# Performance work log

Hardware: AMD Instinct MI355X
Metric: run time of the kernel (lower is better)

The kernel has to match this reference:

```python
import jax, jax.numpy as jnp
import numpy as np

C = 256
NH, NL, NP_ = 8, 3, 4
HD = C // NH
NLAYERS = 6


def sine_pos(H, W, num_feats=128, temperature=10000.0, eps=1e-6):
    # mmdet SinePositionalEncoding with normalize=True and an all-zero padding mask:
    # cumsum of ones -> (i+1), normalized by last element (H or W) * 2*pi.
    scale = 2.0 * np.pi
    y = (jnp.arange(1, H + 1, dtype=jnp.float32) / (H + eps)) * scale
    x = (jnp.arange(1, W + 1, dtype=jnp.float32) / (W + eps)) * scale
    d = jnp.arange(num_feats, dtype=jnp.float32)
    dim_t = temperature ** (2.0 * jnp.floor(d / 2.0) / num_feats)

    def interleave(p):  # p: (n, num_feats) -> sin on even dims, cos on odd dims, interleaved
        return jnp.stack([jnp.sin(p[:, 0::2]), jnp.cos(p[:, 1::2])], axis=-1).reshape(p.shape[0], -1)

    py = interleave(y[:, None] / dim_t)  # (H, num_feats)
    px = interleave(x[:, None] / dim_t)  # (W, num_feats)
    pos = jnp.concatenate([jnp.broadcast_to(py[:, None, :], (H, W, num_feats)),
                           jnp.broadcast_to(px[None, :, :], (H, W, num_feats))], axis=-1)
    return pos.reshape(H * W, 2 * num_feats)


def ref_points(H, W):
    # normalized pixel centers, (x, y) order, shape (H*W, 2)
    ry = (jnp.arange(H, dtype=jnp.float32) + 0.5) / H
    rx = (jnp.arange(W, dtype=jnp.float32) + 0.5) / W
    gy, gx = jnp.meshgrid(ry, rx, indexing='ij')
    return jnp.stack([gx.ravel(), gy.ravel()], axis=-1)


def ln(x, w, b, eps=1e-5):
    m = x.mean(-1, keepdims=True)
    v = x.var(-1, keepdims=True)
    return (x - m) / jnp.sqrt(v + eps) * w + b


def gnorm(x, w, b, groups=32, eps=1e-5):
    B, Ch, H, W = x.shape
    xg = x.reshape(B, groups, Ch // groups, H, W)
    m = xg.mean((2, 3, 4), keepdims=True)
    v = xg.var((2, 3, 4), keepdims=True)
    xg = (xg - m) / jnp.sqrt(v + eps)
    return xg.reshape(B, Ch, H, W) * w[None, :, None, None] + b[None, :, None, None]


def conv3x3(x, w):
    return jax.lax.conv_general_dilated(x, w, (1, 1), 'SAME',
                                        dimension_numbers=('NCHW', 'OIHW', 'NCHW'))


def ms_deform(value, shapes, loc, aw):
    # value (B,S,NH,HD); loc (B,L,NH,NL,NP,2) normalized [0,1]; aw (B,L,NH,NL,NP)
    # Matches F.grid_sample(..., align_corners=False, padding_mode='zeros').
    B, S, nH, hd = value.shape
    Lq, nP = loc.shape[1], loc.shape[4]
    out = jnp.zeros((B, Lq, nH, hd), value.dtype)
    start = 0
    for lvl, (H, W) in enumerate(shapes):
        v = value[:, start:start + H * W].transpose(0, 2, 1, 3)  # (B,nH,HW,hd)
        start += H * W
        l = loc[:, :, :, lvl]                 # (B,Lq,nH,nP,2)
        px = l[..., 0] * W - 0.5
        py = l[..., 1] * H - 0.5
        x0 = jnp.floor(px); y0 = jnp.floor(py)
        lx = px - x0; ly = py - y0
        x0i = x0.astype(jnp.int32); y0i = y0.astype(jnp.int32)

        def tw(w_):  # (B,Lq,nH,nP) -> (B,nH,Lq*nP,1)
            return w_.transpose(0, 2, 1, 3).reshape(B, nH, Lq * nP, 1)

        def gather(xi, yi):
            valid = ((xi >= 0) & (xi < W) & (yi >= 0) & (yi < H)).astype(value.dtype)
            idx = jnp.clip(yi, 0, H - 1) * W + jnp.clip(xi, 0, W - 1)
            idx = idx.transpose(0, 2, 1, 3).reshape(B, nH, Lq * nP)
            g = jnp.take_along_axis(v, idx[..., None], axis=2)  # (B,nH,Lq*nP,hd)
            return g * tw(valid)

        samp = (gather(x0i, y0i) * tw((1 - lx) * (1 - ly))
                + gather(x0i + 1, y0i) * tw(lx * (1 - ly))
                + gather(x0i, y0i + 1) * tw((1 - lx) * ly)
                + gather(x0i + 1, y0i + 1) * tw(lx * ly))
        samp = samp.reshape(B, nH, Lq, nP, hd)
        out = out + jnp.einsum('bqhp,bhqpd->bqhd', aw[:, :, :, lvl], samp)
    return out.reshape(B, Lq, nH * hd)


def _forward(feat0, feat1, feat2, in0_w, in0_b, in1_w, in1_b, in2_w, in2_b,
             off_w, off_b, aw_w, aw_b, vp_w, vp_b, op_w, op_b,
             n1_w, n1_b, ff1_w, ff1_b, ff2_w, ff2_b, n2_w, n2_b,
             fn_w, fn_b, lat_w, lat_b, out_w, gnw, gnb):
    feats = [feat0, feat1, feat2]
    in_ws = [in0_w, in1_w, in2_w]; in_bs = [in0_b, in1_b, in2_b]
    B = feat0.shape[0]
    mlvl = [jnp.einsum('oi,bihw->bohw', w, f) + b[None, :, None, None]
            for f, w, b in zip(feats, in_ws, in_bs)]
    shapes = [(f.shape[2], f.shape[3]) for f in mlvl]
    src = jnp.concatenate([f.reshape(B, C, -1).transpose(0, 2, 1) for f in mlvl], axis=1)  # (B,L,C)
    pos = jnp.concatenate([sine_pos(H, W) for (H, W) in shapes], axis=0)[None]  # (1,L,C)
    ref = jnp.concatenate([ref_points(H, W) for (H, W) in shapes], axis=0)      # (L,2)
    L = ref.shape[0]
    ref = jnp.broadcast_to(ref[None, :, None, :], (B, L, NL, 2))
    norm = jnp.array([[w_, h_] for (h_, w_) in shapes], dtype=src.dtype)  # (NL,2) = (W,H)
    for i in range(NLAYERS):
        q = src + pos
        off = (q @ off_w[i].T + off_b[i]).reshape(B, L, NH, NL, NP_, 2)
        aw = jax.nn.softmax((q @ aw_w[i].T + aw_b[i]).reshape(B, L, NH, NL * NP_), axis=-1)
        aw = aw.reshape(B, L, NH, NL, NP_)
        value = (src @ vp_w[i].T + vp_b[i]).reshape(B, L, NH, HD)
        loc = ref[:, :, None, :, None, :] + off / norm[None, None, None, :, None, :]
        attn = ms_deform(value, shapes, loc, aw) @ op_w[i].T + op_b[i]
        src = ln(src + attn, n1_w[i], n1_b[i])
        ff = jax.nn.relu(src @ ff1_w[i].T + ff1_b[i]) @ ff2_w[i].T + ff2_b[i]
        src = ln(src + ff, n2_w[i], n2_b[i])
    src = ln(src, fn_w, fn_b)
    mems, s = [], 0
    for (H, W) in shapes:
        mems.append(src[:, s:s + H * W].transpose(0, 2, 1).reshape(B, C, H, W))
        s += H * W
    mf = jnp.einsum('oi,bihw->bohw', lat_w, mems[0]) + lat_b[None, :, None, None]
    for i in range(3):
        mf = jax.nn.relu(gnorm(conv3x3(mf, out_w[i]), gnw[i], gnb[i]))
    return (mf, mems[0], mems[1], mems[2])


def setup_inputs():
    ks = iter(jax.random.split(jax.random.key(0), 64))

    def rn(shape, s=0.02):
        return jax.random.normal(next(ks), shape, dtype=jnp.float32) * s

    return dict(
        feat0=rn((1, 256, 64, 64), 1.0),
        feat1=rn((1, 512, 32, 32), 1.0),
        feat2=rn((1, 1024, 16, 16), 1.0),
        in0_w=rn((256, 256)), in0_b=rn((256,)),
        in1_w=rn((256, 512)), in1_b=rn((256,)),
        in2_w=rn((256, 1024)), in2_b=rn((256,)),
        off_w=rn((6, 192, 256), 0.002), off_b=rn((6, 192), 0.5),
        aw_w=rn((6, 96, 256)), aw_b=jnp.zeros((6, 96), jnp.float32),
        vp_w=rn((6, 256, 256)), vp_b=rn((6, 256)),
        op_w=rn((6, 256, 256)), op_b=rn((6, 256)),
        n1_w=jnp.ones((6, 256), jnp.float32), n1_b=jnp.zeros((6, 256), jnp.float32),
        ff1_w=rn((6, 1024, 256)), ff1_b=rn((6, 1024)),
        ff2_w=rn((6, 256, 1024)), ff2_b=rn((6, 256)),
        n2_w=jnp.ones((6, 256), jnp.float32), n2_b=jnp.zeros((6, 256), jnp.float32),
        fn_w=jnp.ones((256,), jnp.float32), fn_b=jnp.zeros((256,), jnp.float32),
        lat_w=rn((256, 256)), lat_b=rn((256,)),
        out_w=rn((3, 256, 256, 3, 3)),
        gnw=jnp.ones((3, 256), jnp.float32), gnb=jnp.zeros((3, 256), jnp.float32),
    )


def reference(feat0, feat1, feat2, in0_w, in0_b, in1_w, in1_b, in2_w, in2_b,
              off_w, off_b, aw_w, aw_b, vp_w, vp_b, op_w, op_b,
              n1_w, n1_b, ff1_w, ff1_b, ff2_w, ff2_b, n2_w, n2_b,
              fn_w, fn_b, lat_w, lat_b, out_w, gnw, gnb):
    return _forward(feat0, feat1, feat2, in0_w, in0_b, in1_w, in1_b, in2_w, in2_b,
                    off_w, off_b, aw_w, aw_b, vp_w, vp_b, op_w, op_b,
                    n1_w, n1_b, ff1_w, ff1_b, ff2_w, ff2_b, n2_w, n2_b,
                    fn_w, fn_b, lat_w, lat_b, out_w, gnw, gnb)
```

## Files before the change

### kernel.cpp

```cpp
#include <hip/hip_runtime.h>
#include <math.h>

#define LTOT 5376

typedef __attribute__((ext_vector_type(8))) __bf16 bf16x8;
typedef __attribute__((ext_vector_type(4))) float f32x4;
typedef __attribute__((ext_vector_type(8))) unsigned short us8;
typedef __attribute__((ext_vector_type(4))) unsigned short us4;

static __device__ __forceinline__ float4 ld4(const float* p) { return *(const float4*)p; }

static __device__ __forceinline__ unsigned short f2bf(float f) {
    unsigned int u = __float_as_uint(f);
    return (unsigned short)((u + 0x7fffu + ((u >> 16) & 1u)) >> 16);
}
static __device__ __forceinline__ float bf2f(unsigned short s) {
    return __uint_as_float(((unsigned int)s) << 16);
}

static __device__ __forceinline__ void gl16(const unsigned short* g, unsigned short* l) {
    __builtin_amdgcn_global_load_lds(
        (const __attribute__((address_space(1))) unsigned int*)g,
        (__attribute__((address_space(3))) unsigned int*)l, 16, 0, 0);
}

template<int OMODE, bool RELU>
__global__ __launch_bounds__(256) void bgemm_k(
    const unsigned short* __restrict__ A,
    const unsigned short* __restrict__ B,
    const float* __restrict__ bias,
    float* __restrict__ C1,
    unsigned short* __restrict__ C2,
    int M, int N, int K)
{
    __shared__ unsigned short As[2][64 * 64];
    __shared__ unsigned short Bs[2][64 * 64];
    const int tid  = threadIdx.x;
    const int m0   = blockIdx.y * 64;
    const int n0   = blockIdx.x * 64;
    const int wave = tid >> 6;
    const int lane = tid & 63;
    const int wm   = (wave >> 1) * 32;
    const int wn   = (wave & 1) * 32;
    const int fr   = lane & 15;
    const int ko   = lane >> 4;

    const int q0 = tid, q1 = tid + 256;
    const int r0 = q0 >> 3, c0v = (q0 & 7) ^ (r0 & 7);
    const int r1 = q1 >> 3, c1v = (q1 & 7) ^ (r1 & 7);
    const unsigned short* a0 = A + (size_t)(m0 + r0) * K + (c0v << 3);
    const unsigned short* a1 = A + (size_t)(m0 + r1) * K + (c1v << 3);
    int bn0 = n0 + r0; if (bn0 > N - 1) bn0 = N - 1;
    int bn1 = n0 + r1; if (bn1 > N - 1) bn1 = N - 1;
    const unsigned short* b0 = B + (size_t)bn0 * K + (c0v << 3);
    const unsigned short* b1 = B + (size_t)bn1 * K + (c1v << 3);
    const int wb = wave << 9;

    f32x4 acc[2][2] = {};

    auto stage = [&](int buf, int kof) {
        gl16(a0 + kof, &As[buf][wb]);
        gl16(a1 + kof, &As[buf][2048 + wb]);
        gl16(b0 + kof, &Bs[buf][wb]);
        gl16(b1 + kof, &Bs[buf][2048 + wb]);
    };

    const int nt = K >> 6;
    stage(0, 0);
    __syncthreads();
    int buf = 0;
    for (int t = 0; t < nt; t++) {
        if (t + 1 < nt) stage(buf ^ 1, (t + 1) << 6);
        #pragma unroll
        for (int sub = 0; sub < 2; sub++) {
            bf16x8 af[2], bfr[2];
            const int kk = (sub << 2) + ko;
            #pragma unroll
            for (int i = 0; i < 2; i++) {
                int r = wm + i * 16 + fr;
                af[i] = *(const bf16x8*)&As[buf][(r << 6) + ((kk ^ (r & 7)) << 3)];
                int c = wn + i * 16 + fr;
                bfr[i] = *(const bf16x8*)&Bs[buf][(c << 6) + ((kk ^ (c & 7)) << 3)];
            }
            #pragma unroll
            for (int i = 0; i < 2; i++)
                #pragma unroll
                for (int j = 0; j < 2; j++)
                    acc[i][j] = __builtin_amdgcn_mfma_f32_16x16x32_bf16(af[i], bfr[j], acc[i][j], 0, 0, 0);
        }
        __syncthreads();
        buf ^= 1;
    }

    #pragma unroll
    for (int j = 0; j < 2; j++) {
        int col = n0 + wn + j * 16 + fr;
        if (col >= N) continue;
        float cb = bias[col];
        #pragma unroll
        for (int i = 0; i < 2; i++) {
            #pragma unroll
            for (int r = 0; r < 4; r++) {
                int row = m0 + wm + i * 16 + ko * 4 + r;
                float v = acc[i][j][r] + cb;
                if (RELU) v = fmaxf(v, 0.f);
                size_t off = (size_t)row * N + col;
                if (OMODE == 0) C1[off] = v;
                else if (OMODE == 1) C2[off] = f2bf(v);
                else { C1[off] = v; C2[off] = f2bf(v); }
            }
        }
    }
}

__global__ void cvtall_k(const float* __restrict__ s0, const float* __restrict__ s1,
                         const float* __restrict__ s2, const float* __restrict__ s3,
                         const float* __restrict__ s4, const float* __restrict__ s5,
                         const float* __restrict__ s6, const float* __restrict__ s7,
                         unsigned short* __restrict__ d)
{
    int i = blockIdx.x * blockDim.x + threadIdx.x;
    if (i >= 1114112) return;
    const float* s; int off;
    if      (i <   98304) { s = s0; off = 0; }
    else if (i <  196608) { s = s1; off = 98304; }
    else if (i <  589824) { s = s2; off = 196608; }
    else if (i <  983040) { s = s3; off = 589824; }
    else if (i <  999424) { s = s4; off = 983040; }
    else if (i < 1032192) { s = s5; off = 999424; }
    else if (i < 1097728) { s = s6; off = 1032192; }
    else                  { s = s7; off = 1097728; }
    float4 v = ld4(&s[(size_t)(i - off) << 2]);
    us4 r = { f2bf(v.x), f2bf(v.y), f2bf(v.z), f2bf(v.w) };
    *(us4*)&d[(size_t)i << 2] = r;
}

__global__ void cvtT_k(const float* __restrict__ src, unsigned short* __restrict__ dst, int Ci, int P)
{
    __shared__ float t[32][33];
    int c0 = blockIdx.y * 32, p0 = blockIdx.x * 32;
    int x = threadIdx.x, y = threadIdx.y;
    for (int i = y; i < 32; i += 8)
        t[i][x] = src[(size_t)(c0 + i) * P + p0 + x];
    __syncthreads();
    for (int i = y; i < 32; i += 8)
        dst[(size_t)(p0 + i) * Ci + c0 + x] = f2bf(t[x][i]);
}

__global__ void pack_oa_k(const float* __restrict__ off_w, const float* __restrict__ off_b,
                          const float* __restrict__ aw_w,  const float* __restrict__ aw_b,
                          unsigned short* __restrict__ w_oa, float* __restrict__ b_oa)
{
    int idx = blockIdx.x * blockDim.x + threadIdx.x;
    if (idx >= 6 * 288 * 256) return;
    int i = idx / 73728;
    int r = idx - i * 73728;
    int n = r >> 8;
    int k = r & 255;
    float v = (n < 192) ? off_w[((size_t)i * 192 + n) * 256 + k]
                        : aw_w[((size_t)i * 96 + (n - 192)) * 256 + k];
    w_oa[idx] = f2bf(v);
    if (k == 0)
        b_oa[i * 288 + n] = (n < 192) ? off_b[i * 192 + n] : aw_b[i * 96 + (n - 192)];
}

__global__ void wconv_k(const float* __restrict__ out_w, unsigned short* __restrict__ wcb)
{
    int idx = blockIdx.x * blockDim.x + threadIdx.x;
    if (idx >= 3 * 589824) return;
    int c   = idx / 589824;
    int r   = idx - c * 589824;
    int icc = r / 73728;
    int r2  = r - icc * 73728;
    int oc  = r2 / 288;
    int r3  = r2 - oc * 288;
    int tap = r3 >> 5;
    int sl  = r3 & 31;
    int ic  = icc * 32 + (((sl >> 3) ^ ((oc >> 1) & 3)) << 3) + (sl & 7);
    wcb[idx] = f2bf(out_w[(((size_t)(c * 256 + oc)) * 256 + ic) * 9 + tap]);
}

__global__ void posenc_k(float* __restrict__ pos)
{
    int idx = blockIdx.x * blockDim.x + threadIdx.x;
    if (idx >= LTOT * 128) return;
    int l = idx >> 7;
    int pr = idx & 127;
    int half = pr >> 6;
    int j = pr & 63;
    int HW, sh, p;
    if (l < 4096)      { HW = 64; sh = 6; p = l; }
    else if (l < 5120) { HW = 32; sh = 5; p = l - 4096; }
    else               { HW = 16; sh = 4; p = l - 5120; }
    int y = p >> sh;
    int x = p & (HW - 1);
    float T = powf(10000.f, (float)j * (1.f / 64.f));
    float coord = (half == 0) ? (float)(y + 1) : (float)(x + 1);
    float v = coord / ((float)HW + 1e-6f) * 6.283185307179586f;
    float arg = v / T;
    size_t base = (size_t)l * 256 + half * 128 + (j << 1);
    pos[base]     = sinf(arg);
    pos[base + 1] = cosf(arg);
}

__global__ void addb_k(const float* __restrict__ a, const float* __restrict__ b,
                       unsigned short* __restrict__ o, int n4)
{
    int i = blockIdx.x * blockDim.x + threadIdx.x;
    if (i >= n4) return;
    float4 x = ld4(&a[(size_t)i << 2]);
    float4 y = ld4(&b[(size_t)i << 2]);
    us4 r = { f2bf(x.x + y.x), f2bf(x.y + y.y), f2bf(x.z + y.z), f2bf(x.w + y.w) };
    *(us4*)&o[(size_t)i << 2] = r;
}

__global__ __launch_bounds__(256) void msdef_k(
    const unsigned short* __restrict__ valb, const float* __restrict__ oab,
    unsigned short* __restrict__ out)
{
    __shared__ float sw[8 * 288];
    const int tid = threadIdx.x;
    const int bl = blockIdx.x;
    #pragma unroll
    for (int id = tid; id < 576; id += 256)
        ((float4*)sw)[id] = ((const float4*)(oab + (size_t)bl * 2304))[id];
    __syncthreads();

    const int p = tid >> 5;
    const int t = tid & 31;
    const int l = bl * 8 + p;
    const int h = t >> 2;
    const int co = (t & 3) << 3;
    const float* mo = sw + p * 288;

    float aw_r[12];
    {
        const float* sc = mo + 192 + h * 12;
        float mx = -1e30f;
        #pragma unroll
        for (int j = 0; j < 12; j++) { aw_r[j] = sc[j]; mx = fmaxf(mx, aw_r[j]); }
        float su = 0.f;
        #pragma unroll
        for (int j = 0; j < 12; j++) { aw_r[j] = expf(aw_r[j] - mx); su += aw_r[j]; }
        float inv = 1.f / su;
        #pragma unroll
        for (int j = 0; j < 12; j++) aw_r[j] *= inv;
    }

    float rx, ry;
    {
        int HW, sh, q;
        if (l < 4096)      { HW = 64; sh = 6; q = l; }
        else if (l < 5120) { HW = 32; sh = 5; q = l - 4096; }
        else               { HW = 16; sh = 4; q = l - 5120; }
        int y = q >> sh;
        int x = q & (HW - 1);
        rx = (x + 0.5f) / (float)HW;
        ry = (y + 0.5f) / (float)HW;
    }

    const int starts[3] = {0, 4096, 5120};
    const int dims[3]   = {64, 32, 16};
    float acc[8] = {};
    #pragma unroll
    for (int s = 0; s < 3; s++) {
        const int D = dims[s];
        const int st = starts[s];
        #pragma unroll
        for (int pt = 0; pt < 4; pt++) {
            float a  = aw_r[(s << 2) + pt];
            float px = rx * D + mo[h * 24 + (s << 3) + (pt << 1)]     - 0.5f;
            float py = ry * D + mo[h * 24 + (s << 3) + (pt << 1) + 1] - 0.5f;
            float x0f = floorf(px), y0f = floorf(py);
            float lx = px - x0f, ly = py - y0f;
            int x0 = (int)x0f, y0 = (int)y0f;
            float w00 = a * (1.f - lx) * (1.f - ly);
            float w10 = a * lx * (1.f - ly);
            float w01 = a * (1.f - lx) * ly;
            float w11 = a * lx * ly;
            #pragma unroll
            for (int cy = 0; cy < 2; cy++) {
                int yi = y0 + cy;
                if (yi < 0 || yi >= D) continue;
                #pragma unroll
                for (int cx = 0; cx < 2; cx++) {
                    int xi = x0 + cx;
                    if (xi < 0 || xi >= D) continue;
                    float w = cy ? (cx ? w11 : w01) : (cx ? w10 : w00);
                    us8 v = *(const us8*)&valb[((size_t)(st + yi * D + xi) << 8) + (h << 5) + co];
                    #pragma unroll
                    for (int e = 0; e < 8; e++)
                        acc[e] = fmaf(w, bf2f(v[e]), acc[e]);
                }
            }
        }
    }
    us8 r;
    #pragma unroll
    for (int e = 0; e < 8; e++) r[e] = f2bf(acc[e]);
    *(us8*)&out[((size_t)l << 8) + (h << 5) + co] = r;
}

template<bool HAS_ADD, bool HAS_POS>
__global__ __launch_bounds__(256) void ln_k(float* __restrict__ src, const float* __restrict__ add,
                                            const float* __restrict__ w, const float* __restrict__ b,
                                            unsigned short* __restrict__ outb,
                                            const float* __restrict__ posf,
                                            unsigned short* __restrict__ qbout)
{
    int row = blockIdx.x * 4 + (threadIdx.x >> 6);
    int lane = threadIdx.x & 63;
    size_t base = (size_t)row * 256 + (lane << 2);
    float4 x = ld4(&src[base]);
    if (HAS_ADD) {
        float4 a = ld4(&add[base]);
        x.x += a.x; x.y += a.y; x.z += a.z; x.w += a.w;
    }
    float s = x.x + x.y + x.z + x.w;
    #pragma unroll
    for (int o = 32; o > 0; o >>= 1) s += __shfl_xor(s, o, 64);
    float m = s * (1.f / 256.f);
    float d0 = x.x - m, d1 = x.y - m, d2 = x.z - m, d3 = x.w - m;
    float v = d0 * d0 + d1 * d1 + d2 * d2 + d3 * d3;
    #pragma unroll
    for (int o = 32; o > 0; o >>= 1) v += __shfl_xor(v, o, 64);
    float rs = rsqrtf(v * (1.f / 256.f) + 1e-5f);
    float4 wv = ld4(&w[lane << 2]);
    float4 bv = ld4(&b[lane << 2]);
    float4 o4;
    o4.x = d0 * rs * wv.x + bv.x;
    o4.y = d1 * rs * wv.y + bv.y;
    o4.z = d2 * rs * wv.z + bv.z;
    o4.w = d3 * rs * wv.w + bv.w;
    *(float4*)&src[base] = o4;
    us4 r = { f2bf(o4.x), f2bf(o4.y), f2bf(o4.z), f2bf(o4.w) };
    *(us4*)&outb[base] = r;
    if (HAS_POS) {
        float4 p4 = ld4(&posf[base]);
        us4 q = { f2bf(o4.x + p4.x), f2bf(o4.y + p4.y), f2bf(o4.z + p4.z), f2bf(o4.w + p4.w) };
        *(us4*)&qbout[base] = q;
    }
}

__global__ void tr_k(const float* __restrict__ src, float* __restrict__ dst, int HW)
{
    __shared__ float t[32][33];
    int p0 = blockIdx.x * 32, c0 = blockIdx.y * 32;
    int x = threadIdx.x, y = threadIdx.y;
    for (int i = y; i < 32; i += 8)
        t[i][x] = src[(size_t)(p0 + i) * 256 + c0 + x];
    __syncthreads();
    for (int i = y; i < 32; i += 8)
        dst[(size_t)(c0 + i) * HW + p0 + x] = t[x][i];
}

__global__ __launch_bounds__(256) void conv3b_k(const unsigned short* __restrict__ inb,
                                                const unsigned short* __restrict__ wcb,
                                                float* __restrict__ out)
{
    __shared__ __align__(16) unsigned char smem[43776];
    unsigned short* sIn = (unsigned short*)smem;
    unsigned short* sW  = (unsigned short*)(smem + 6912);
    float* sO = (float*)smem;

    const int tid = threadIdx.x;
    const int mb = blockIdx.x;
    const int y0 = (mb >> 2) << 2;
    const int x0 = (mb & 3) << 4;
    const int oc0 = blockIdx.y << 6;
    const int wave = tid >> 6, lane = tid & 63;
    const int wm = (wave >> 1) * 32, wn = (wave & 1) * 32;
    const int fr = lane & 15, ko = lane >> 4;

    f32x4 acc[2][2] = {};

    for (int icc = 0; icc < 8; icc++) {
        __syncthreads();
        #pragma unroll
        for (int id = tid; id < 432; id += 256) {
            int pxi = id >> 2, ch = id & 3;
            int r = pxi / 18, s = pxi - r * 18;
            int gy = y0 - 1 + r, gx = x0 - 1 + s;
            us8 v = {};
            if (gy >= 0 && gy < 64 && gx >= 0 && gx < 64)
                v = *(const us8*)&inb[((size_t)(gy * 64 + gx) << 8) + (icc << 5) + (ch << 3)];
            *(us8*)&sIn[(pxi << 5) + ((ch ^ ((s >> 1) & 3)) << 3)] = v;
        }
        const unsigned short* wsrc = wcb + (((size_t)icc * 256 + oc0) * 9 << 5);
        #pragma unroll
        for (int id = tid; id < 2304; id += 256)
            *(us8*)&sW[id << 3] = *(const us8*)&wsrc[id << 3];
        __syncthreads();

        #pragma unroll
        for (int tap = 0; tap < 9; tap++) {
            const int ky = tap / 3, kx = tap - ky * 3;
            bf16x8 a[2], b[2];
            #pragma unroll
            for (int i = 0; i < 2; i++) {
                int px = wm + i * 16 + fr;
                int r = (px >> 4) + ky;
                int s = (px & 15) + kx;
                a[i] = *(const bf16x8*)&sIn[(((r * 18 + s)) << 5) + ((ko ^ ((s >> 1) & 3)) << 3)];
            }
            #pragma unroll
            for (int j = 0; j < 2; j++) {
                int oc = wn + j * 16 + fr;
                b[j] = *(const bf16x8*)&sW[(((oc * 9) + tap) << 5) + ((ko ^ ((oc >> 1) & 3)) << 3)];
            }
            #pragma unroll
            for (int i = 0; i < 2; i++)
                #pragma unroll
                for (int j = 0; j < 2; j++)
                    acc[i][j] = __builtin_amdgcn_mfma_f32_16x16x32_bf16(a[i], b[j], acc[i][j], 0, 0, 0);
        }
    }

    __syncthreads();
    #pragma unroll
    for (int i = 0; i < 2; i++)
        #pragma unroll
        for (int j = 0; j < 2; j++) {
            int oc = wn + j * 16 + fr;
            int pxb = wm + i * 16 + ko * 4;
            *(f32x4*)&sO[oc * 68 + pxb] = acc[i][j];
        }
    __syncthreads();
    {
        int oc_r = tid >> 2, yy = tid & 3;
        float* dst = &out[(size_t)(oc0 + oc_r) * 4096 + (y0 + yy) * 64 + x0];
        const float* srcl = &sO[oc_r * 68 + yy * 16];
        #pragma unroll
        for (int q = 0; q < 4; q++)
            *(float4*)&dst[q * 4] = *(const float4*)&srcl[q * 4];
    }
}

__global__ __launch_bounds__(256) void gnstats_k(const float* __restrict__ x, float* __restrict__ st)
{
    int g = blockIdx.x;
    const float* p = x + (size_t)g * 8 * 4096;
    float s = 0.f, ss = 0.f;
    for (int i = threadIdx.x * 4; i < 32768; i += 1024) {
        float4 v = ld4(&p[i]);
        s  += v.x + v.y + v.z + v.w;
        ss += v.x * v.x + v.y * v.y + v.z * v.z + v.w * v.w;
    }
    #pragma unroll
    for (int o = 32; o > 0; o >>= 1) {
        s  += __shfl_xor(s, o, 64);
        ss += __shfl_xor(ss, o, 64);
    }
    __shared__ float rs[4], rss[4];
    int wid = threadIdx.x >> 6;
    if ((threadIdx.x & 63) == 0) { rs[wid] = s; rss[wid] = ss; }
    __syncthreads();
    if (threadIdx.x == 0) {
        float S = rs[0] + rs[1] + rs[2] + rs[3];
        float SS = rss[0] + rss[1] + rss[2] + rss[3];
        float m = S * (1.f / 32768.f);
        float var = SS * (1.f / 32768.f) - m * m;
        st[g * 2] = m;
        st[g * 2 + 1] = rsqrtf(var + 1e-5f);
    }
}

__global__ void gnapply_b_k(const float* __restrict__ x, const float* __restrict__ st,
                            const float* __restrict__ w, const float* __restrict__ b,
                            unsigned short* __restrict__ o)
{
    int i = blockIdx.x * blockDim.x + threadIdx.x;
    if (i >= 262144) return;
    int c = i >> 10;
    int g = c >> 3;
    int px0 = (i & 1023) << 2;
    float m = st[g * 2], rs = st[g * 2 + 1];
    float sw = w[c], sb = b[c];
    float4 v = ld4(&x[(size_t)i << 2]);
    float r0 = fmaxf((v.x - m) * rs * sw + sb, 0.f);
    float r1 = fmaxf((v.y - m) * rs * sw + sb, 0.f);
    float r2 = fmaxf((v.z - m) * rs * sw + sb, 0.f);
    float r3 = fmaxf((v.w - m) * rs * sw + sb, 0.f);
    o[(size_t)(px0 + 0) * 256 + c] = f2bf(r0);
    o[(size_t)(px0 + 1) * 256 + c] = f2bf(r1);
    o[(size_t)(px0 + 2) * 256 + c] = f2bf(r2);
    o[(size_t)(px0 + 3) * 256 + c] = f2bf(r3);
}

__global__ void gnapply_f_k(const float* __restrict__ x, const float* __restrict__ st,
                            const float* __restrict__ w, const float* __restrict__ b,
                            float* __restrict__ o)
{
    int i = blockIdx.x * blockDim.x + threadIdx.x;
    if (i >= 262144) return;
    int c = i >> 10;
    int g = c >> 3;
    float m = st[g * 2], rs = st[g * 2 + 1];
    float sw = w[c], sb = b[c];
    float4 v = ld4(&x[(size_t)i << 2]);
    float4 r;
    r.x = fmaxf((v.x - m) * rs * sw + sb, 0.f);
    r.y = fmaxf((v.y - m) * rs * sw + sb, 0.f);
    r.z = fmaxf((v.z - m) * rs * sw + sb, 0.f);
    r.w = fmaxf((v.w - m) * rs * sw + sb, 0.f);
    *(float4*)&o[(size_t)i << 2] = r;
}

extern "C" void kernel_launch(void* const* d_in, const int* in_sizes, int n_in,
                              void* d_out, int out_size, void* d_ws, size_t ws_size,
                              hipStream_t stream)
{
    (void)in_sizes; (void)n_in; (void)out_size; (void)ws_size;
    const float* feat0 = (const float*)d_in[0];
    const float* feat1 = (const float*)d_in[1];
    const float* feat2 = (const float*)d_in[2];
    const float* in0_w = (const float*)d_in[3];
    const float* in0_b = (const float*)d_in[4];
    const float* in1_w = (const float*)d_in[5];
    const float* in1_b = (const float*)d_in[6];
    const float* in2_w = (const float*)d_in[7];
    const float* in2_b = (const float*)d_in[8];
    const float* off_w = (const float*)d_in[9];
    const float* off_b = (const float*)d_in[10];
    const float* aw_w  = (const float*)d_in[11];
    const float* aw_b  = (const float*)d_in[12];
    const float* vp_w  = (const float*)d_in[13];
    const float* vp_b  = (const float*)d_in[14];
    const float* op_w  = (const float*)d_in[15];
    const float* op_b  = (const float*)d_in[16];
    const float* n1_w  = (const float*)d_in[17];
    const float* n1_b  = (const float*)d_in[18];
    const float* ff1_w = (const float*)d_in[19];
    const float* ff1_b = (const float*)d_in[20];
    const float* ff2_w = (const float*)d_in[21];
    const float* ff2_b = (const float*)d_in[22];
    const float* n2_w  = (const float*)d_in[23];
    const float* n2_b  = (const float*)d_in[24];
    const float* fn_w  = (const float*)d_in[25];
    const float* fn_b  = (const float*)d_in[26];
    const float* lat_w = (const float*)d_in[27];
    const float* lat_b = (const float*)d_in[28];
    const float* out_w = (const float*)d_in[29];
    const float* gnw   = (const float*)d_in[30];
    const float* gnb   = (const float*)d_in[31];
    float* out = (float*)d_out;

    float* ws     = (float*)d_ws;
    float* src    = ws;
    float* pos    = src  + 1376256;
    float* tmp    = pos  + 1376256;
    float* valbuf = tmp  + 1376256;
    float* oab    = valbuf + 1376256;
    float* stats  = oab  + 1548288;
    float* boa    = stats + 64;
    float* pong   = pos;

    unsigned short* valb = (unsigned short*)valbuf;
    unsigned short* latb = (unsigned short*)(valbuf + 688128);

    unsigned short* ub = (unsigned short*)(boa + 1728);
    unsigned short* srcb  = ub; ub += 1376256;
    unsigned short* qbb   = ub; ub += 1376256;
    unsigned short* msdb  = ub; ub += 1376256;
    unsigned short* ffhb  = ub; ub += 5505024;
    unsigned short* w_oa  = ub; ub += 442368;
    unsigned short* w_vp  = ub; ub += 393216;
    unsigned short* w_op  = ub; ub += 393216;
    unsigned short* w_ff1 = ub; ub += 1572864;
    unsigned short* w_ff2 = ub; ub += 1572864;
    unsigned short* w_in0 = ub; ub += 65536;
    unsigned short* w_in1 = ub; ub += 131072;
    unsigned short* w_in2 = ub; ub += 262144;
    unsigned short* w_lat = ub; ub += 65536;
    unsigned short* wcb   = ub; ub += 1769472;

    unsigned short* fT0 = ffhb;
    unsigned short* fT1 = ffhb + 1048576;
    unsigned short* fT2 = ffhb + 1572864;
    unsigned short* pingb = qbb;

    pack_oa_k<<<1728, 256, 0, stream>>>(off_w, off_b, aw_w, aw_b, w_oa, boa);
    wconv_k<<<6912, 256, 0, stream>>>(out_w, wcb);
    cvtall_k<<<4352, 256, 0, stream>>>(vp_w, op_w, ff1_w, ff2_w, in0_w, in1_w, in2_w, lat_w, w_vp);
    cvtT_k<<<dim3(128, 8), dim3(32, 8), 0, stream>>>(feat0, fT0, 256, 4096);
    cvtT_k<<<dim3(32, 16), dim3(32, 8), 0, stream>>>(feat1, fT1, 512, 1024);
    cvtT_k<<<dim3(8, 32),  dim3(32, 8), 0, stream>>>(feat2, fT2, 1024, 256);
    posenc_k<<<2688, 256, 0, stream>>>(pos);

    bgemm_k<2,false><<<dim3(4,64), 256, 0, stream>>>(fT0, w_in0, in0_b, src,            srcb,            4096, 256, 256);
    bgemm_k<2,false><<<dim3(4,16), 256, 0, stream>>>(fT1, w_in1, in1_b, src + 4096*256, srcb + 4096*256, 1024, 256, 512);
    bgemm_k<2,false><<<dim3(4,4),  256, 0, stream>>>(fT2, w_in2, in2_b, src + 5120*256, srcb + 5120*256, 256,  256, 1024);
    addb_k<<<1344, 256, 0, stream>>>(src, pos, qbb, 344064);

    for (int i = 0; i < 6; i++) {
        bgemm_k<0,false><<<dim3(5,84), 256, 0, stream>>>(qbb,  w_oa + i*73728, boa + i*288, oab, nullptr, 5376, 288, 256);
        bgemm_k<1,false><<<dim3(4,84), 256, 0, stream>>>(srcb, w_vp + i*65536, vp_b + i*256, nullptr, valb, 5376, 256, 256);
        msdef_k<<<672, 256, 0, stream>>>(valb, oab, msdb);
        bgemm_k<0,false><<<dim3(4,84), 256, 0, stream>>>(msdb, w_op + i*65536, op_b + i*256, tmp, nullptr, 5376, 256, 256);
        ln_k<true,false><<<1344, 256, 0, stream>>>(src, tmp, n1_w + i*256, n1_b + i*256, srcb, nullptr, nullptr);
        bgemm_k<1,true ><<<dim3(16,84),256, 0, stream>>>(srcb, w_ff1 + i*262144, ff1_b + i*1024, nullptr, ffhb, 5376, 1024, 256);
        bgemm_k<0,false><<<dim3(4,84), 256, 0, stream>>>(ffhb, w_ff2 + i*262144, ff2_b + i*256, tmp, nullptr, 5376, 256, 1024);
        if (i < 5)
            ln_k<true,true><<<1344, 256, 0, stream>>>(src, tmp, n2_w + i*256, n2_b + i*256, srcb, pos, qbb);
        else
            ln_k<true,false><<<1344, 256, 0, stream>>>(src, tmp, n2_w + i*256, n2_b + i*256, srcb, nullptr, nullptr);
    }
    ln_k<false,false><<<1344, 256, 0, stream>>>(src, nullptr, fn_w, fn_b, srcb, nullptr, nullptr);

    tr_k<<<dim3(128,8), dim3(32,8), 0, stream>>>(src,           out + 1048576, 4096);
    tr_k<<<dim3(32,8),  dim3(32,8), 0, stream>>>(src + 1048576, out + 2097152, 1024);
    tr_k<<<dim3(8,8),   dim3(32,8), 0, stream>>>(src + 1310720, out + 2359296, 256);

    bgemm_k<1,false><<<dim3(4,64), 256, 0, stream>>>(srcb, w_lat, lat_b, nullptr, latb, 4096, 256, 256);

    conv3b_k<<<dim3(64,4), 256, 0, stream>>>(latb, wcb, pong);
    gnstats_k<<<32, 256, 0, stream>>>(pong, stats);
    gnapply_b_k<<<1024, 256, 0, stream>>>(pong, stats, gnw, gnb, pingb);

    conv3b_k<<<dim3(64,4), 256, 0, stream>>>(pingb, wcb + 589824, pong);
    gnstats_k<<<32, 256, 0, stream>>>(pong, stats);
    gnapply_b_k<<<1024, 256, 0, stream>>>(pong, stats, gnw + 256, gnb + 256, pingb);

    conv3b_k<<<dim3(64,4), 256, 0, stream>>>(pingb, wcb + 1179648, pong);
    gnstats_k<<<32, 256, 0, stream>>>(pong, stats);
    gnapply_f_k<<<1024, 256, 0, stream>>>(pong, stats, gnw + 512, gnb + 512, out);
}
```

Measured before the change: 659.1 us.

## Triple-buffer GEMM pipeline and merge projection launches into combined kernels

```diff
diff --git a/kernel.cpp b/kernel.cpp
--- a/kernel.cpp
+++ b/kernel.cpp
@@ -24,20 +24,16 @@
         (__attribute__((address_space(3))) unsigned int*)l, 16, 0, 0);
 }
 
-template<int OMODE, bool RELU>
-__global__ __launch_bounds__(256) void bgemm_k(
+__device__ __forceinline__ void gemm_core(
     const unsigned short* __restrict__ A,
     const unsigned short* __restrict__ B,
     const float* __restrict__ bias,
-    float* __restrict__ C1,
-    unsigned short* __restrict__ C2,
-    int M, int N, int K)
-{
-    __shared__ unsigned short As[2][64 * 64];
-    __shared__ unsigned short Bs[2][64 * 64];
+    float* __restrict__ C1, unsigned short* __restrict__ C2,
+    const float* __restrict__ posf, unsigned short* __restrict__ qb,
+    unsigned short* As, unsigned short* Bs,
+    int m0, int mo0, int n0, int N, int K, int omode, int relu)
+{
     const int tid  = threadIdx.x;
-    const int m0   = blockIdx.y * 64;
-    const int n0   = blockIdx.x * 64;
     const int wave = tid >> 6;
     const int lane = tid & 63;
     const int wm   = (wave >> 1) * 32;
@@ -57,20 +53,26 @@
     const int wb = wave << 9;
 
     f32x4 acc[2][2] = {};
-
-    auto stage = [&](int buf, int kof) {
-        gl16(a0 + kof, &As[buf][wb]);
-        gl16(a1 + kof, &As[buf][2048 + wb]);
-        gl16(b0 + kof, &Bs[buf][wb]);
-        gl16(b1 + kof, &Bs[buf][2048 + wb]);
+    const int nt = K >> 6;
+
+    auto stage = [&](int buf, int t) {
+        const int kof = t << 6;
+        gl16(a0 + kof, As + buf * 4096 + wb);
+        gl16(a1 + kof, As + buf * 4096 + 2048 + wb);
+        gl16(b0 + kof, Bs + buf * 4096 + wb);
+        gl16(b1 + kof, Bs + buf * 4096 + 2048 + wb);
     };
 
-    const int nt = K >> 6;
     stage(0, 0);
-    __syncthreads();
-    int buf = 0;
+    stage(1, 1);
+    asm volatile("s_waitcnt vmcnt(4)" ::: "memory");
+    __builtin_amdgcn_s_barrier();
+    __builtin_amdgcn_sched_barrier(0);
+
     for (int t = 0; t < nt; t++) {
-        if (t + 1 < nt) stage(buf ^ 1, (t + 1) << 6);
+        if (t + 2 < nt) stage((t + 2) % 3, t + 2);
+        const unsigned short* Ab = As + (t % 3) * 4096;
+        const unsigned short* Bb = Bs + (t % 3) * 4096;
         #pragma unroll
         for (int sub = 0; sub < 2; sub++) {
             bf16x8 af[2], bfr[2];
@@ -78,9 +80,9 @@
             #pragma unroll
             for (int i = 0; i < 2; i++) {
                 int r = wm + i * 16 + fr;
-                af[i] = *(const bf16x8*)&As[buf][(r << 6) + ((kk ^ (r & 7)) << 3)];
+                af[i] = *(const bf16x8*)&Ab[(r << 6) + ((kk ^ (r & 7)) << 3)];
                 int c = wn + i * 16 + fr;
-                bfr[i] = *(const bf16x8*)&Bs[buf][(c << 6) + ((kk ^ (c & 7)) << 3)];
+                bfr[i] = *(const bf16x8*)&Bb[(c << 6) + ((kk ^ (c & 7)) << 3)];
             }
             #pragma unroll
             for (int i = 0; i < 2; i++)
@@ -88,8 +90,12 @@
                 for (int j = 0; j < 2; j++)
                     acc[i][j] = __builtin_amdgcn_mfma_f32_16x16x32_bf16(af[i], bfr[j], acc[i][j], 0, 0, 0);
         }
-        __syncthreads();
-        buf ^= 1;
+        if (t + 1 < nt) {
+            if (t + 2 < nt) asm volatile("s_waitcnt vmcnt(4) lgkmcnt(0)" ::: "memory");
+            else            asm volatile("s_waitcnt vmcnt(0) lgkmcnt(0)" ::: "memory");
+            __builtin_amdgcn_s_barrier();
+            __builtin_amdgcn_sched_barrier(0);
+        }
     }
 
     #pragma unroll
@@ -101,16 +107,60 @@
         for (int i = 0; i < 2; i++) {
             #pragma unroll
             for (int r = 0; r < 4; r++) {
-                int row = m0 + wm + i * 16 + ko * 4 + r;
+                int row = mo0 + wm + i * 16 + ko * 4 + r;
                 float v = acc[i][j][r] + cb;
-                if (RELU) v = fmaxf(v, 0.f);
+                if (relu) v = fmaxf(v, 0.f);
                 size_t off = (size_t)row * N + col;
-                if (OMODE == 0) C1[off] = v;
-                else if (OMODE == 1) C2[off] = f2bf(v);
-                else { C1[off] = v; C2[off] = f2bf(v); }
+                if (omode == 0)      C1[off] = v;
+                else if (omode == 1) C2[off] = f2bf(v);
+                else if (omode == 2) { C1[off] = v; C2[off] = f2bf(v); }
+                else { C1[off] = v; C2[off] = f2bf(v); qb[off] = f2bf(v + posf[off]); }
             }
         }
     }
+}
+
+__global__ __launch_bounds__(256) void bgemm_k(
+    const unsigned short* __restrict__ A, const unsigned short* __restrict__ B,
+    const float* __restrict__ bias, float* __restrict__ C1, unsigned short* __restrict__ C2,
+    int N, int K, int omode, int relu)
+{
+    __shared__ unsigned short As[3 * 4096], Bs[3 * 4096];
+    int m = blockIdx.y * 64;
+    gemm_core(A, B, bias, C1, C2, nullptr, nullptr, As, Bs, m, m, blockIdx.x * 64, N, K, omode, relu);
+}
+
+__global__ __launch_bounds__(256) void oavp_k(
+    const unsigned short* __restrict__ qbb, const unsigned short* __restrict__ woa,
+    const float* __restrict__ boa, float* __restrict__ oab,
+    const unsigned short* __restrict__ srcb, const unsigned short* __restrict__ wvp,
+    const float* __restrict__ bvp, unsigned short* __restrict__ valb)
+{
+    __shared__ unsigned short As[3 * 4096], Bs[3 * 4096];
+    const int bx = blockIdx.x;
+    const int m = blockIdx.y * 64;
+    if (bx < 5)
+        gemm_core(qbb,  woa, boa, oab, nullptr, nullptr, nullptr, As, Bs, m, m, bx * 64, 288, 256, 0, 0);
+    else
+        gemm_core(srcb, wvp, bvp, nullptr, valb, nullptr, nullptr, As, Bs, m, m, (bx - 5) * 64, 256, 256, 1, 0);
+}
+
+__global__ __launch_bounds__(256) void inproj_k(
+    const unsigned short* __restrict__ fT0, const unsigned short* __restrict__ w0, const float* __restrict__ b0,
+    const unsigned short* __restrict__ fT1, const unsigned short* __restrict__ w1, const float* __restrict__ b1,
+    const unsigned short* __restrict__ fT2, const unsigned short* __restrict__ w2, const float* __restrict__ b2,
+    float* __restrict__ src, unsigned short* __restrict__ srcb,
+    const float* __restrict__ posf, unsigned short* __restrict__ qbb)
+{
+    __shared__ unsigned short As[3 * 4096], Bs[3 * 4096];
+    const int by = blockIdx.y;
+    const int n0 = blockIdx.x * 64;
+    if (by < 64)
+        gemm_core(fT0, w0, b0, src, srcb, posf, qbb, As, Bs, by * 64, by * 64, n0, 256, 256, 3, 0);
+    else if (by < 80)
+        gemm_core(fT1, w1, b1, src, srcb, posf, qbb, As, Bs, (by - 64) * 64, 4096 + (by - 64) * 64, n0, 256, 512, 3, 0);
+    else
+        gemm_core(fT2, w2, b2, src, srcb, posf, qbb, As, Bs, (by - 80) * 64, 5120 + (by - 80) * 64, n0, 256, 1024, 3, 0);
 }
 
 __global__ void cvtall_k(const float* __restrict__ s0, const float* __restrict__ s1,
@@ -201,17 +251,6 @@
     size_t base = (size_t)l * 256 + half * 128 + (j << 1);
     pos[base]     = sinf(arg);
     pos[base + 1] = cosf(arg);
-}
-
-__global__ void addb_k(const float* __restrict__ a, const float* __restrict__ b,
-                       unsigned short* __restrict__ o, int n4)
-{
-    int i = blockIdx.x * blockDim.x + threadIdx.x;
-    if (i >= n4) return;
-    float4 x = ld4(&a[(size_t)i << 2]);
-    float4 y = ld4(&b[(size_t)i << 2]);
-    us4 r = { f2bf(x.x + y.x), f2bf(x.y + y.y), f2bf(x.z + y.z), f2bf(x.w + y.w) };
-    *(us4*)&o[(size_t)i << 2] = r;
 }
 
 __global__ __launch_bounds__(256) void msdef_k(
@@ -587,19 +626,17 @@
     cvtT_k<<<dim3(8, 32),  dim3(32, 8), 0, stream>>>(feat2, fT2, 1024, 256);
     posenc_k<<<2688, 256, 0, stream>>>(pos);
 
-    bgemm_k<2,false><<<dim3(4,64), 256, 0, stream>>>(fT0, w_in0, in0_b, src,            srcb,            4096, 256, 256);
-    bgemm_k<2,false><<<dim3(4,16), 256, 0, stream>>>(fT1, w_in1, in1_b, src + 4096*256, srcb + 4096*256, 1024, 256, 512);
-    bgemm_k<2,false><<<dim3(4,4),  256, 0, stream>>>(fT2, w_in2, in2_b, src + 5120*256, srcb + 5120*256, 256,  256, 1024);
-    addb_k<<<1344, 256, 0, stream>>>(src, pos, qbb, 344064);
+    inproj_k<<<dim3(4, 84), 256, 0, stream>>>(fT0, w_in0, in0_b, fT1, w_in1, in1_b,
+                                              fT2, w_in2, in2_b, src, srcb, pos, qbb);
 
     for (int i = 0; i < 6; i++) {
-        bgemm_k<0,false><<<dim3(5,84), 256, 0, stream>>>(qbb,  w_oa + i*73728, boa + i*288, oab, nullptr, 5376, 288, 256);
-        bgemm_k<1,false><<<dim3(4,84), 256, 0, stream>>>(srcb, w_vp + i*65536, vp_b + i*256, nullptr, valb, 5376, 256, 256);
+        oavp_k<<<dim3(9, 84), 256, 0, stream>>>(qbb, w_oa + i*73728, boa + i*288, oab,
+                                                srcb, w_vp + i*65536, vp_b + i*256, valb);
         msdef_k<<<672, 256, 0, stream>>>(valb, oab, msdb);
-        bgemm_k<0,false><<<dim3(4,84), 256, 0, stream>>>(msdb, w_op + i*65536, op_b + i*256, tmp, nullptr, 5376, 256, 256);
+        bgemm_k<<<dim3(4, 84), 256, 0, stream>>>(msdb, w_op + i*65536, op_b + i*256, tmp, nullptr, 256, 256, 0, 0);
         ln_k<true,false><<<1344, 256, 0, stream>>>(src, tmp, n1_w + i*256, n1_b + i*256, srcb, nullptr, nullptr);
-        bgemm_k<1,true ><<<dim3(16,84),256, 0, stream>>>(srcb, w_ff1 + i*262144, ff1_b + i*1024, nullptr, ffhb, 5376, 1024, 256);
-        bgemm_k<0,false><<<dim3(4,84), 256, 0, stream>>>(ffhb, w_ff2 + i*262144, ff2_b + i*256, tmp, nullptr, 5376, 256, 1024);
+        bgemm_k<<<dim3(16, 84), 256, 0, stream>>>(srcb, w_ff1 + i*262144, ff1_b + i*1024, nullptr, ffhb, 1024, 256, 1, 1);
+        bgemm_k<<<dim3(4, 84), 256, 0, stream>>>(ffhb, w_ff2 + i*262144, ff2_b + i*256, tmp, nullptr, 256, 1024, 0, 0);
         if (i < 5)
             ln_k<true,true><<<1344, 256, 0, stream>>>(src, tmp, n2_w + i*256, n2_b + i*256, srcb, pos, qbb);
         else
@@ -611,7 +648,7 @@
     tr_k<<<dim3(32,8),  dim3(32,8), 0, stream>>>(src + 1048576, out + 2097152, 1024);
     tr_k<<<dim3(8,8),   dim3(32,8), 0, stream>>>(src + 1310720, out + 2359296, 256);
 
-    bgemm_k<1,false><<<dim3(4,64), 256, 0, stream>>>(srcb, w_lat, lat_b, nullptr, latb, 4096, 256, 256);
+    bgemm_k<<<dim3(4, 64), 256, 0, stream>>>(srcb, w_lat, lat_b, nullptr, latb, 256, 256, 1, 0);
 
     conv3b_k<<<dim3(64,4), 256, 0, stream>>>(latb, wcb, pong);
     gnstats_k<<<32, 256, 0, stream>>>(pong, stats);
```

After: 642.3 us. 2.5% less time.
